# Kernel tuning notes

Hardware: AMD Instinct MI355X
Metric: run time of the kernel (lower is better)

Reference implementation:

```python
import jax, jax.numpy as jnp
import numpy as np

N = 50000

def gcn_conv(x, src, dst, W, b):
    # PyG GCNConv: h = x @ W; symmetric norm with self-loops; out = Ahat h + b
    h = x @ W  # [N, F]
    e = src.shape[0]
    deg = jax.ops.segment_sum(jnp.ones((e,), h.dtype), dst, num_segments=N) + 1.0  # +1 self-loop
    dinv = jax.lax.rsqrt(deg)  # deg >= 1 so finite
    norm = dinv[src] * dinv[dst]  # [E]
    agg = jax.ops.segment_sum(h[src] * norm[:, None], dst, num_segments=N)
    agg = agg + h * (dinv * dinv)[:, None]  # self-loop contribution
    return agg + b


def setup_inputs() -> dict:
    key = jax.random.key(0)
    ks = jax.random.split(key, 12)
    E = 400000
    x = jax.random.normal(ks[0], (N, 768), dtype=jnp.float32)
    edge_index = jax.random.randint(ks[1], (2, E), 0, N, dtype=jnp.int32)
    dims = [(768, 1536), (1536, 768), (768, 384), (384, 192), (192, 5)]
    inp = {"x": x, "edge_index": edge_index}
    for i, (fi, fo) in enumerate(dims):
        s = 1.0 / np.sqrt(fi)
        inp[f"W{i+1}"] = jax.random.uniform(ks[2 + 2 * i], (fi, fo), jnp.float32, -s, s)
        inp[f"b{i+1}"] = jnp.zeros((fo,), jnp.float32)
    return inp


def reference(x, edge_index, W1, b1, W2, b2, W3, b3, W4, b4, W5, b5):
    src, dst = edge_index[0], edge_index[1]
    h = x
    for W, b in [(W1, b1), (W2, b2), (W3, b3), (W4, b4)]:
        h = jax.nn.relu(gcn_conv(h, src, dst, W, b))
        # F.dropout with training=False is identity (eval mode)
    out = gcn_conv(h, src, dst, W5, b5)
    return (h, out)
```

## Files before the change

### kernel.cpp

```cpp
#include <hip/hip_runtime.h>
#include <stdint.h>

typedef unsigned short u16;
typedef unsigned int   u32;

#define NN 50000
#define NE 400000

typedef __bf16 bf16x8 __attribute__((ext_vector_type(8)));
typedef u16    u16x8  __attribute__((ext_vector_type(8)));
typedef float  f32x4  __attribute__((ext_vector_type(4)));

__device__ __forceinline__ float bf2f(u16 b) {
  union { u32 u; float f; } v; v.u = ((u32)b) << 16; return v.f;
}
__device__ __forceinline__ u16 f2bf(float f) {
  union { float f; u32 u; } v; v.f = f;
  u32 r = v.u + 0x7fffu + ((v.u >> 16) & 1u);
  return (u16)(r >> 16);
}


__global__ void zero_int_kernel(int* __restrict__ p, int n) {
  int i = blockIdx.x * blockDim.x + threadIdx.x;
  if (i < n) p[i] = 0;
}

__global__ void count_deg_kernel(const int* __restrict__ dst, int* __restrict__ deg, int e) {
  int i = blockIdx.x * blockDim.x + threadIdx.x;
  if (i < e) atomicAdd(&deg[dst[i]], 1);
}

__global__ void dinv_kernel(const int* __restrict__ deg, float* __restrict__ dinv, int n) {
  int i = blockIdx.x * blockDim.x + threadIdx.x;
  if (i < n) dinv[i] = rsqrtf((float)deg[i] + 1.0f);
}

__global__ __launch_bounds__(1024) void scan_kernel(const int* __restrict__ counts,
                                                    int* __restrict__ offsets, int n) {
  __shared__ int wsums[17];
  __shared__ int carry;
  int tid = threadIdx.x;
  int lane = tid & 63, wid = tid >> 6;
  if (tid == 0) carry = 0;
  __syncthreads();
  for (int base = 0; base < n; base += 1024) {
    int i = base + tid;
    int v = (i < n) ? counts[i] : 0;
    int s = v;
    #pragma unroll
    for (int off = 1; off < 64; off <<= 1) {
      int t = __shfl_up(s, off, 64);
      if (lane >= off) s += t;
    }
    if (lane == 63) wsums[wid] = s;
    __syncthreads();
    if (tid == 0) {
      int a = 0;
      #pragma unroll
      for (int w = 0; w < 16; ++w) { int t = wsums[w]; wsums[w] = a; a += t; }
      wsums[16] = a;
    }
    __syncthreads();
    if (i < n) offsets[i] = carry + wsums[wid] + s - v;
    __syncthreads();
    if (tid == 0) carry += wsums[16];
    __syncthreads();
  }
  if (tid == 0) offsets[n] = carry;
}

__global__ void csr_fill_kernel(const int* __restrict__ src, const int* __restrict__ dst,
                                const int* __restrict__ offsets, int* __restrict__ cursor,
                                const float* __restrict__ dinv,
                                int2* __restrict__ csr_pack, int e) {
  int i = blockIdx.x * blockDim.x + threadIdx.x;
  if (i < e) {
    int s = src[i], d = dst[i];
    int pos = offsets[d] + atomicAdd(&cursor[d], 1);
    float nr = dinv[s] * dinv[d];
    csr_pack[pos] = make_int2(s, __float_as_int(nr));
  }
}

__global__ void f2bf_kernel(const float* __restrict__ in, u16* __restrict__ out, int n) {
  int i = blockIdx.x * blockDim.x + threadIdx.x;
  if (i < n) out[i] = f2bf(in[i]);
}

__global__ void wt_kernel(const float* __restrict__ W, u16* __restrict__ Wt, int K, int N) {
  int i = blockIdx.x * blockDim.x + threadIdx.x;
  if (i < K * N) {
    int k = i / N;
    int n2 = i - k * N;
    Wt[n2 * K + k] = f2bf(W[i]);
  }
}


template<int G, bool HAS_BIAS, bool RELU, bool OUT_BF, bool OUT_F32>
__global__ __launch_bounds__(256) void agg8_kernel(
    const u16* __restrict__ g, const int* __restrict__ rowptr,
    const int2* __restrict__ csr_pack,
    const float* __restrict__ dinv, const float* __restrict__ bias,
    u16* __restrict__ outb, float* __restrict__ outf)
{
  constexpr int F = G * 8;
  int idx = blockIdx.x * blockDim.x + threadIdx.x;
  if (idx >= NN * G) return;
  int v = idx / G;
  int g8 = idx - v * G;
  const u16* base = g + g8 * 8;

  float acc[8];
  #pragma unroll
  for (int k = 0; k < 8; ++k) acc[k] = 0.f;

  int e0 = rowptr[v], e1 = rowptr[v + 1];
  int e = e0;
  for (; e + 3 < e1; e += 4) {
    int2 p0 = csr_pack[e];
    int2 p1 = csr_pack[e + 1];
    int2 p2 = csr_pack[e + 2];
    int2 p3 = csr_pack[e + 3];
    u16x8 r0 = *(const u16x8*)(base + (size_t)p0.x * F);
    u16x8 r1 = *(const u16x8*)(base + (size_t)p1.x * F);
    u16x8 r2 = *(const u16x8*)(base + (size_t)p2.x * F);
    u16x8 r3 = *(const u16x8*)(base + (size_t)p3.x * F);
    float n0 = __int_as_float(p0.y), n1 = __int_as_float(p1.y);
    float n2 = __int_as_float(p2.y), n3 = __int_as_float(p3.y);
    #pragma unroll
    for (int k = 0; k < 8; ++k) acc[k] += n0 * bf2f(r0[k]);
    #pragma unroll
    for (int k = 0; k < 8; ++k) acc[k] += n1 * bf2f(r1[k]);
    #pragma unroll
    for (int k = 0; k < 8; ++k) acc[k] += n2 * bf2f(r2[k]);
    #pragma unroll
    for (int k = 0; k < 8; ++k) acc[k] += n3 * bf2f(r3[k]);
  }
  for (; e < e1; ++e) {
    int2 p0 = csr_pack[e];
    u16x8 r0 = *(const u16x8*)(base + (size_t)p0.x * F);
    float n0 = __int_as_float(p0.y);
    #pragma unroll
    for (int k = 0; k < 8; ++k) acc[k] += n0 * bf2f(r0[k]);
  }

  float sv = dinv[v]; sv *= sv;
  u16x8 sr = *(const u16x8*)(base + (size_t)v * F);
  float vals[8];
  #pragma unroll
  for (int k = 0; k < 8; ++k) {
    float val = acc[k] + sv * bf2f(sr[k]);
    if (HAS_BIAS) val += bias[g8 * 8 + k];
    if (RELU) val = fmaxf(val, 0.f);
    vals[k] = val;
  }
  if (OUT_BF) {
    u16x8 ob;
    #pragma unroll
    for (int k = 0; k < 8; ++k) ob[k] = f2bf(vals[k]);
    *(u16x8*)(outb + (size_t)v * F + g8 * 8) = ob;
  }
  if (OUT_F32) {
    f32x4 o0, o1;
    #pragma unroll
    for (int k = 0; k < 4; ++k) { o0[k] = vals[k]; o1[k] = vals[4 + k]; }
    float* op = outf + (size_t)v * F + g8 * 8;
    *(f32x4*)op = o0;
    *(f32x4*)(op + 4) = o1;
  }
}

__global__ void agg_small_kernel(const u16* __restrict__ g, const int* __restrict__ rowptr,
                                 const int2* __restrict__ csr_pack,
                                 const float* __restrict__ dinv, const float* __restrict__ bias,
                                 float* __restrict__ out, int n, int F) {
  int idx = blockIdx.x * blockDim.x + threadIdx.x;
  if (idx >= n * F) return;
  int v = idx / F;
  int f = idx - v * F;
  float acc = 0.f;
  int e1 = rowptr[v + 1];
  for (int e = rowptr[v]; e < e1; ++e) {
    int2 p = csr_pack[e];
    acc += __int_as_float(p.y) * bf2f(g[p.x * F + f]);
  }
  float dv = dinv[v];
  out[idx] = acc + dv * dv * bf2f(g[v * F + f]) + bias[f];
}

#define WAIT_VMCNT4 0x0F74
#define WAIT_VMCNT0 0x0F70

__device__ __forceinline__ void gl_lds16(const void* g, void* l) {
  __builtin_amdgcn_global_load_lds((const __attribute__((address_space(1))) void*)g,
                                   (__attribute__((address_space(3))) void*)l, 16, 0, 0);
}


template<bool BIAS_RELU>
__global__ __launch_bounds__(512, 2) void gemm256_kernel(
    const u16* __restrict__ A, const u16* __restrict__ Bt,
    u16* __restrict__ C, const float* __restrict__ bias,
    int M, int N, int K)
{
  __shared__ __align__(16) u16 sA[2][2][256 * 32];
  __shared__ __align__(16) u16 sB[2][2][256 * 32];

  int gm = (M + 255) >> 8;
  int gn = (N + 255) >> 8;
  int bid = blockIdx.x;
  int xcd = bid & 7;
  int t = bid >> 3;
  int trow = t / gn;
  int bn_i = t - trow * gn;
  int rowt = trow * 8 + xcd;
  if (rowt >= gm) return;
  int bm = rowt << 8, bn = bn_i << 8;

  int tid = threadIdx.x;
  int wid = tid >> 6, lane = tid & 63;
  int wm = wid >> 2, wn = wid & 3;
  int row16 = lane & 15, q = lane >> 4;

  int sr = tid >> 2;
  int sq_log = ((tid & 3) - ((tid >> 3) & 3)) & 3;
  int ar0 = min(bm + sr, M - 1);
  int ar1 = min(bm + 128 + sr, M - 1);
  int br0 = min(bn + sr, N - 1);
  int br1 = min(bn + 128 + sr, N - 1);
  const u16* Ag0 = A + (size_t)ar0 * K + sq_log * 8;
  const u16* Ag1 = A + (size_t)ar1 * K + sq_log * 8;
  const u16* Bg0 = Bt + (size_t)br0 * K + sq_log * 8;
  const u16* Bg1 = Bt + (size_t)br1 * K + sq_log * 8;

  f32x4 acc[8][4];
  #pragma unroll
  for (int m = 0; m < 8; ++m)
    #pragma unroll
    for (int n = 0; n < 4; ++n)
      acc[m][n] = (f32x4){0.f, 0.f, 0.f, 0.f};

  auto stageA = [&](int nb, int h, int ko) {
    gl_lds16(Ag0 + ko, &sA[nb][h][tid * 8]);
    gl_lds16(Ag1 + ko, &sA[nb][h][4096 + tid * 8]);
  };
  auto stageB = [&](int nb, int h, int ko) {
    gl_lds16(Bg0 + ko, &sB[nb][h][tid * 8]);
    gl_lds16(Bg1 + ko, &sB[nb][h][4096 + tid * 8]);
  };

  stageA(0, 0, 0);
  stageB(0, 0, 0);
  stageA(0, 1, 32);
  stageB(0, 1, 32);
  __builtin_amdgcn_s_waitcnt(WAIT_VMCNT4);
  __builtin_amdgcn_s_barrier();

  const int KT = K >> 6;
  int perm = (q + (row16 >> 1)) & 3;
  int arow = (wm * 128 + row16) * 32 + perm * 8;
  int brow = (wn * 64 + row16) * 32 + perm * 8;

  for (int kt = 0; kt < KT; ++kt) {
    int buf = kt & 1, nb = buf ^ 1;
    bool pf = (kt + 1 < KT);
    int ko = (kt + 1) * 64;

    bf16x8 af[4], bfr[4];

    #pragma unroll
    for (int m = 0; m < 4; ++m) af[m] = *(const bf16x8*)&sA[buf][0][arow + m * 512];
    #pragma unroll
    for (int n = 0; n < 4; ++n) bfr[n] = *(const bf16x8*)&sB[buf][0][brow + n * 512];
    if (pf) stageA(nb, 0, ko);
    __builtin_amdgcn_s_setprio(1);
    #pragma unroll
    for (int m = 0; m < 4; ++m)
      #pragma unroll
      for (int n = 0; n < 4; ++n)
        acc[m][n] = __builtin_amdgcn_mfma_f32_16x16x32_bf16(af[m], bfr[n], acc[m][n], 0, 0, 0);
    __builtin_amdgcn_s_setprio(0);

    #pragma unroll
    for (int m = 0; m < 4; ++m) af[m] = *(const bf16x8*)&sA[buf][0][arow + (m + 4) * 512];
    if (pf) stageB(nb, 0, ko);
    __builtin_amdgcn_s_setprio(1);
    #pragma unroll
    for (int m = 0; m < 4; ++m)
      #pragma unroll
      for (int n = 0; n < 4; ++n)
        acc[m + 4][n] = __builtin_amdgcn_mfma_f32_16x16x32_bf16(af[m], bfr[n], acc[m + 4][n], 0, 0, 0);
    __builtin_amdgcn_s_setprio(0);

    if (pf) __builtin_amdgcn_s_waitcnt(WAIT_VMCNT4);
    else    __builtin_amdgcn_s_waitcnt(WAIT_VMCNT0);
    __builtin_amdgcn_s_barrier();

    #pragma unroll
    for (int m = 0; m < 4; ++m) af[m] = *(const bf16x8*)&sA[buf][1][arow + m * 512];
    #pragma unroll
    for (int n = 0; n < 4; ++n) bfr[n] = *(const bf16x8*)&sB[buf][1][brow + n * 512];
    if (pf) stageA(nb, 1, ko + 32);
    __builtin_amdgcn_s_setprio(1);
    #pragma unroll
    for (int m = 0; m < 4; ++m)
      #pragma unroll
      for (int n = 0; n < 4; ++n)
        acc[m][n] = __builtin_amdgcn_mfma_f32_16x16x32_bf16(af[m], bfr[n], acc[m][n], 0, 0, 0);
    __builtin_amdgcn_s_setprio(0);

    #pragma unroll
    for (int m = 0; m < 4; ++m) af[m] = *(const bf16x8*)&sA[buf][1][arow + (m + 4) * 512];
    if (pf) stageB(nb, 1, ko + 32);
    __builtin_amdgcn_s_setprio(1);
    #pragma unroll
    for (int m = 0; m < 4; ++m)
      #pragma unroll
      for (int n = 0; n < 4; ++n)
        acc[m + 4][n] = __builtin_amdgcn_mfma_f32_16x16x32_bf16(af[m], bfr[n], acc[m + 4][n], 0, 0, 0);
    __builtin_amdgcn_s_setprio(0);

    if (pf) {
      __builtin_amdgcn_s_waitcnt(WAIT_VMCNT4);
      __builtin_amdgcn_s_barrier();
    }
  }

  #pragma unroll
  for (int m = 0; m < 8; ++m) {
    int rbase = bm + wm * 128 + m * 16 + q * 4;
    #pragma unroll
    for (int n = 0; n < 4; ++n) {
      int col = bn + wn * 64 + n * 16 + row16;
      if (col < N) {
        float bv = BIAS_RELU ? bias[col] : 0.f;
        #pragma unroll
        for (int r = 0; r < 4; ++r) {
          int gr = rbase + r;
          if (gr < M) {
            float val = acc[m][n][r];
            if (BIAS_RELU) { val += bv; val = fmaxf(val, 0.f); }
            C[(size_t)gr * N + col] = f2bf(val);
          }
        }
      }
    }
  }
}

static inline int gemm256_grid(int M, int N) {
  int gm = (M + 255) / 256;
  int gn = (N + 255) / 256;
  int rows_per_xcd = (gm + 7) / 8;
  return rows_per_xcd * 8 * gn;
}


#define BM 128
#define BN 128
#define BK 32

template<bool BIAS_RELU>
__global__ __launch_bounds__(256, 4) void gemm_bt_kernel(
    const u16* __restrict__ A, const u16* __restrict__ Bt,
    u16* __restrict__ C, const float* __restrict__ bias,
    int M, int N, int K)
{
  __shared__ __align__(16) u16 As[2][BM * BK];
  __shared__ __align__(16) u16 Bs[2][BN * BK];
  int gm = (M + BM - 1) / BM;
  int gn = (N + BN - 1) / BN;
  int bid = blockIdx.x;
  int xcd = bid & 7;
  int t = bid >> 3;
  int trow = t / gn;
  int bn_i = t - trow * gn;
  int row = trow * 8 + xcd;
  if (row >= gm) return;
  int bm = row * BM, bn = bn_i * BN;

  int tid = threadIdx.x;
  int wave = tid >> 6, lane = tid & 63;
  int wm = wave & 1, wn = wave >> 1;

  int srow = tid >> 2;
  int sq_log = ((tid & 3) - ((tid >> 3) & 3)) & 3;
  int ar0 = min(bm + srow, M - 1);
  int ar1 = min(bm + 64 + srow, M - 1);
  int br0 = min(bn + srow, N - 1);
  int br1 = min(bn + 64 + srow, N - 1);
  const u16* ag0 = A + (size_t)ar0 * K + sq_log * 8;
  const u16* ag1 = A + (size_t)ar1 * K + sq_log * 8;
  const u16* bg0 = Bt + (size_t)br0 * K + sq_log * 8;
  const u16* bg1 = Bt + (size_t)br1 * K + sq_log * 8;
  int la0 = (wave * 16) * BK;
  int la1 = (64 + wave * 16) * BK;

  f32x4 acc[4][4];
  #pragma unroll
  for (int i = 0; i < 4; ++i)
    #pragma unroll
    for (int j = 0; j < 4; ++j)
      acc[i][j] = (f32x4){0.f, 0.f, 0.f, 0.f};

  int row16 = lane & 15, q = lane >> 4;
  int perm = (q + (row16 >> 1)) & 3;
  int ard = (wm * 64 + row16) * BK + perm * 8;
  int brd = (wn * 64 + row16) * BK + perm * 8;

  const int iters = K / BK;

  gl_lds16(ag0, &As[0][la0]);
  gl_lds16(ag1, &As[0][la1]);
  gl_lds16(bg0, &Bs[0][la0]);
  gl_lds16(bg1, &Bs[0][la1]);

  int buf = 0;
  for (int it = 0; it < iters; ++it) {
    __builtin_amdgcn_s_barrier();
    if (it + 1 < iters) {
      int kn = (it + 1) * BK;
      gl_lds16(ag0 + kn, &As[buf ^ 1][la0]);
      gl_lds16(ag1 + kn, &As[buf ^ 1][la1]);
      gl_lds16(bg0 + kn, &Bs[buf ^ 1][la0]);
      gl_lds16(bg1 + kn, &Bs[buf ^ 1][la1]);
      __builtin_amdgcn_s_waitcnt(WAIT_VMCNT4);
    } else {
      __builtin_amdgcn_s_waitcnt(WAIT_VMCNT0);
    }
    __builtin_amdgcn_s_barrier();

    bf16x8 af[4], bfr[4];
    #pragma unroll
    for (int i = 0; i < 4; ++i) af[i] = *(const bf16x8*)(&As[buf][ard + i * 16 * BK]);
    #pragma unroll
    for (int j = 0; j < 4; ++j) bfr[j] = *(const bf16x8*)(&Bs[buf][brd + j * 16 * BK]);
    #pragma unroll
    for (int i = 0; i < 4; ++i)
      #pragma unroll
      for (int j = 0; j < 4; ++j)
        acc[i][j] = __builtin_amdgcn_mfma_f32_16x16x32_bf16(af[i], bfr[j], acc[i][j], 0, 0, 0);
    buf ^= 1;
  }

  #pragma unroll
  for (int i = 0; i < 4; ++i) {
    int rbase = bm + wm * 64 + i * 16 + q * 4;
    #pragma unroll
    for (int j = 0; j < 4; ++j) {
      int col = bn + wn * 64 + j * 16 + row16;
      if (col < N) {
        float bv = BIAS_RELU ? bias[col] : 0.f;
        #pragma unroll
        for (int r = 0; r < 4; ++r) {
          int gr = rbase + r;
          if (gr < M) {
            float val = acc[i][j][r];
            if (BIAS_RELU) { val += bv; val = fmaxf(val, 0.f); }
            C[(size_t)gr * N + col] = f2bf(val);
          }
        }
      }
    }
  }
}

static inline int gemm_grid(int M, int N) {
  int gm = (M + BM - 1) / BM;
  int gn = (N + BN - 1) / BN;
  int rows_per_xcd = (gm + 7) / 8;
  return rows_per_xcd * gn * 8;
}


extern "C" void kernel_launch(void* const* d_in, const int* in_sizes, int n_in,
                              void* d_out, int out_size, void* d_ws, size_t ws_size,
                              hipStream_t stream) {
  const float* x   = (const float*)d_in[0];
  const int* ei    = (const int*)d_in[1];
  const int* src   = ei;
  const int* dst   = ei + NE;
  const float* W1  = (const float*)d_in[2];
  const float* b1  = (const float*)d_in[3];
  const float* W2  = (const float*)d_in[4];
  const float* b2  = (const float*)d_in[5];
  const float* W3  = (const float*)d_in[6];
  const float* b3  = (const float*)d_in[7];
  const float* W4  = (const float*)d_in[8];
  const float* b4  = (const float*)d_in[9];
  const float* W5  = (const float*)d_in[10];
  const float* b5  = (const float*)d_in[11];
  float* out_h = (float*)d_out;
  float* out_o = (float*)d_out + (size_t)NN * 192;

  char* p = (char*)d_ws;
  auto alloc = [&](size_t bytes) { char* r = p; p += (bytes + 255) & ~(size_t)255; return r; };
  int*   deg      = (int*)alloc((size_t)NN * 4);
  int*   cursor   = (int*)alloc((size_t)NN * 4);
  float* dinv     = (float*)alloc((size_t)NN * 4);
  int*   offs     = (int*)alloc((size_t)(NN + 1) * 4);
  int2*  csr_pack = (int2*)alloc((size_t)NE * 8);
  u16* W1t = (u16*)alloc((size_t)768 * 1536 * 2);
  u16* W2t = (u16*)alloc((size_t)1536 * 768 * 2);
  u16* W3t = (u16*)alloc((size_t)768 * 384 * 2);
  u16* W4t = (u16*)alloc((size_t)384 * 192 * 2);
  u16* W5t = (u16*)alloc((size_t)192 * 5 * 2);
  u16* B0 = (u16*)alloc((size_t)NN * 768 * 2);
  u16* B1 = (u16*)alloc((size_t)NN * 768 * 2);
  u16* B2 = (u16*)alloc((size_t)NN * 1536 * 2);

  u16* xb  = B0;
  u16* a0  = B1;
  u16* h1  = B2;
  u16* g2  = B0;
  u16* h2  = B1;
  u16* g3  = B0;
  u16* h3  = B2;
  u16* g4  = B0;
  u16* h4b = B1;
  u16* g5  = B0;

  const int M = NN;

  zero_int_kernel<<<(NN + 255) / 256, 256, 0, stream>>>(deg, NN);
  zero_int_kernel<<<(NN + 255) / 256, 256, 0, stream>>>(cursor, NN);
  count_deg_kernel<<<(NE + 255) / 256, 256, 0, stream>>>(dst, deg, NE);
  dinv_kernel<<<(NN + 255) / 256, 256, 0, stream>>>(deg, dinv, NN);
  scan_kernel<<<1, 1024, 0, stream>>>(deg, offs, NN);
  csr_fill_kernel<<<(NE + 255) / 256, 256, 0, stream>>>(src, dst, offs, cursor, dinv,
                                                        csr_pack, NE);
  f2bf_kernel<<<((NN * 768) + 255) / 256, 256, 0, stream>>>(x, xb, NN * 768);
  wt_kernel<<<((768 * 1536) + 255) / 256, 256, 0, stream>>>(W1, W1t, 768, 1536);
  wt_kernel<<<((1536 * 768) + 255) / 256, 256, 0, stream>>>(W2, W2t, 1536, 768);
  wt_kernel<<<((768 * 384) + 255) / 256, 256, 0, stream>>>(W3, W3t, 768, 384);
  wt_kernel<<<((384 * 192) + 255) / 256, 256, 0, stream>>>(W4, W4t, 384, 192);
  wt_kernel<<<((192 * 5) + 255) / 256, 256, 0, stream>>>(W5, W5t, 192, 5);

  dim3 blk(256);

  agg8_kernel<96, false, false, true, false><<<(NN * 96 + 255) / 256, blk, 0, stream>>>(
      xb, offs, csr_pack, dinv, nullptr, a0, nullptr);
  gemm256_kernel<true><<<gemm256_grid(M, 1536), 512, 0, stream>>>(
      a0, W1t, h1, b1, M, 1536, 768);

  gemm256_kernel<false><<<gemm256_grid(M, 768), 512, 0, stream>>>(
      h1, W2t, g2, nullptr, M, 768, 1536);
  agg8_kernel<96, true, true, true, false><<<(NN * 96 + 255) / 256, blk, 0, stream>>>(
      g2, offs, csr_pack, dinv, b2, h2, nullptr);

  gemm_bt_kernel<false><<<gemm_grid(M, 384), blk, 0, stream>>>(
      h2, W3t, g3, nullptr, M, 384, 768);
  agg8_kernel<48, true, true, true, false><<<(NN * 48 + 255) / 256, blk, 0, stream>>>(
      g3, offs, csr_pack, dinv, b3, h3, nullptr);

  gemm_bt_kernel<false><<<gemm_grid(M, 192), blk, 0, stream>>>(
      h3, W4t, g4, nullptr, M, 192, 384);
  agg8_kernel<24, true, true, true, true><<<(NN * 24 + 255) / 256, blk, 0, stream>>>(
      g4, offs, csr_pack, dinv, b4, h4b, out_h);

  gemm_bt_kernel<false><<<gemm_grid(M, 5), blk, 0, stream>>>(
      h4b, W5t, g5, nullptr, M, 5, 192);
  agg_small_kernel<<<((NN * 5) + 255) / 256, 256, 0, stream>>>(
      g5, offs, csr_pack, dinv, b5, out_o, NN, 5);
}
```

Baseline: 1.105 ms.

## Restructure GEMM LDS pipeline into 4-stage ring with K=32 steps

Replaces the double-buffered 64-wide K tile (two 32-wide halves per buffer) with a four-slot ring of 32-wide K tiles, prefetching three tiles ahead. This keeps more global-to-LDS loads in flight to hide memory latency. It adds extra barriers around each MFMA group and halves the work per loop iteration, so synchronisation overhead rises. LDS usage per block is unchanged.

Result: slower. 1.137 ms (+2.9%).

```diff
diff --git a/kernel.cpp b/kernel.cpp
--- a/kernel.cpp
+++ b/kernel.cpp
@@ -190,6 +190,7 @@
   out[idx] = acc + dv * dv * bf2f(g[v * F + f]) + bias[f];
 }
 
+#define WAIT_VMCNT8 0x0F78
 #define WAIT_VMCNT4 0x0F74
 #define WAIT_VMCNT0 0x0F70
 
@@ -205,16 +206,16 @@
     u16* __restrict__ C, const float* __restrict__ bias,
     int M, int N, int K)
 {
-  __shared__ __align__(16) u16 sA[2][2][256 * 32];
-  __shared__ __align__(16) u16 sB[2][2][256 * 32];
+  __shared__ __align__(16) u16 sA[4][256 * 32];
+  __shared__ __align__(16) u16 sB[4][256 * 32];
 
   int gm = (M + 255) >> 8;
   int gn = (N + 255) >> 8;
   int bid = blockIdx.x;
   int xcd = bid & 7;
-  int t = bid >> 3;
-  int trow = t / gn;
-  int bn_i = t - trow * gn;
+  int t0 = bid >> 3;
+  int trow = t0 / gn;
+  int bn_i = t0 - trow * gn;
   int rowt = trow * 8 + xcd;
   if (rowt >= gm) return;
   int bm = rowt << 8, bn = bn_i << 8;
@@ -242,90 +243,65 @@
     for (int n = 0; n < 4; ++n)
       acc[m][n] = (f32x4){0.f, 0.f, 0.f, 0.f};
 
-  auto stageA = [&](int nb, int h, int ko) {
-    gl_lds16(Ag0 + ko, &sA[nb][h][tid * 8]);
-    gl_lds16(Ag1 + ko, &sA[nb][h][4096 + tid * 8]);
+  auto stageA = [&](int b, int kt) {
+    gl_lds16(Ag0 + kt * 32, &sA[b][tid * 8]);
+    gl_lds16(Ag1 + kt * 32, &sA[b][4096 + tid * 8]);
   };
-  auto stageB = [&](int nb, int h, int ko) {
-    gl_lds16(Bg0 + ko, &sB[nb][h][tid * 8]);
-    gl_lds16(Bg1 + ko, &sB[nb][h][4096 + tid * 8]);
+  auto stageB = [&](int b, int kt) {
+    gl_lds16(Bg0 + kt * 32, &sB[b][tid * 8]);
+    gl_lds16(Bg1 + kt * 32, &sB[b][4096 + tid * 8]);
   };
 
-  stageA(0, 0, 0);
-  stageB(0, 0, 0);
-  stageA(0, 1, 32);
-  stageB(0, 1, 32);
-  __builtin_amdgcn_s_waitcnt(WAIT_VMCNT4);
+  const int KT = K >> 5;
+
+  stageA(0, 0); stageB(0, 0);
+  stageA(1, 1); stageB(1, 1);
+  stageA(2, 2); stageB(2, 2);
+  __builtin_amdgcn_s_waitcnt(WAIT_VMCNT8);
   __builtin_amdgcn_s_barrier();
 
-  const int KT = K >> 6;
   int perm = (q + (row16 >> 1)) & 3;
   int arow = (wm * 128 + row16) * 32 + perm * 8;
   int brow = (wn * 64 + row16) * 32 + perm * 8;
 
-  for (int kt = 0; kt < KT; ++kt) {
-    int buf = kt & 1, nb = buf ^ 1;
-    bool pf = (kt + 1 < KT);
-    int ko = (kt + 1) * 64;
+  for (int t = 0; t < KT; ++t) {
+    int buf = t & 3;
+    bool pf = (t + 3 < KT);
+    int sb = (t + 3) & 3;
 
     bf16x8 af[4], bfr[4];
 
     #pragma unroll
-    for (int m = 0; m < 4; ++m) af[m] = *(const bf16x8*)&sA[buf][0][arow + m * 512];
-    #pragma unroll
-    for (int n = 0; n < 4; ++n) bfr[n] = *(const bf16x8*)&sB[buf][0][brow + n * 512];
-    if (pf) stageA(nb, 0, ko);
+    for (int i = 0; i < 4; ++i) af[i] = *(const bf16x8*)&sA[buf][arow + i * 512];
+    #pragma unroll
+    for (int n = 0; n < 4; ++n) bfr[n] = *(const bf16x8*)&sB[buf][brow + n * 512];
+    if (pf) stageA(sb, t + 3);
+    __builtin_amdgcn_s_barrier();
     __builtin_amdgcn_s_setprio(1);
     #pragma unroll
-    for (int m = 0; m < 4; ++m)
+    for (int i = 0; i < 4; ++i)
       #pragma unroll
       for (int n = 0; n < 4; ++n)
-        acc[m][n] = __builtin_amdgcn_mfma_f32_16x16x32_bf16(af[m], bfr[n], acc[m][n], 0, 0, 0);
+        acc[i][n] = __builtin_amdgcn_mfma_f32_16x16x32_bf16(af[i], bfr[n], acc[i][n], 0, 0, 0);
     __builtin_amdgcn_s_setprio(0);
-
-    #pragma unroll
-    for (int m = 0; m < 4; ++m) af[m] = *(const bf16x8*)&sA[buf][0][arow + (m + 4) * 512];
-    if (pf) stageB(nb, 0, ko);
+    __builtin_amdgcn_s_barrier();
+
+    #pragma unroll
+    for (int i = 0; i < 4; ++i) af[i] = *(const bf16x8*)&sA[buf][arow + (i + 4) * 512];
+    if (pf) stageB(sb, t + 3);
+    __builtin_amdgcn_s_barrier();
     __builtin_amdgcn_s_setprio(1);
     #pragma unroll
-    for (int m = 0; m < 4; ++m)
+    for (int i = 0; i < 4; ++i)
       #pragma unroll
       for (int n = 0; n < 4; ++n)
-        acc[m + 4][n] = __builtin_amdgcn_mfma_f32_16x16x32_bf16(af[m], bfr[n], acc[m + 4][n], 0, 0, 0);
+        acc[i + 4][n] = __builtin_amdgcn_mfma_f32_16x16x32_bf16(af[i], bfr[n], acc[i + 4][n], 0, 0, 0);
     __builtin_amdgcn_s_setprio(0);
 
-    if (pf) __builtin_amdgcn_s_waitcnt(WAIT_VMCNT4);
-    else    __builtin_amdgcn_s_waitcnt(WAIT_VMCNT0);
-    __builtin_amdgcn_s_barrier();
-
-    #pragma unroll
-    for (int m = 0; m < 4; ++m) af[m] = *(const bf16x8*)&sA[buf][1][arow + m * 512];
-    #pragma unroll
-    for (int n = 0; n < 4; ++n) bfr[n] = *(const bf16x8*)&sB[buf][1][brow + n * 512];
-    if (pf) stageA(nb, 1, ko + 32);
-    __builtin_amdgcn_s_setprio(1);
-    #pragma unroll
-    for (int m = 0; m < 4; ++m)
-      #pragma unroll
-      for (int n = 0; n < 4; ++n)
-        acc[m][n] = __builtin_amdgcn_mfma_f32_16x16x32_bf16(af[m], bfr[n], acc[m][n], 0, 0, 0);
-    __builtin_amdgcn_s_setprio(0);
-
-    #pragma unroll
-    for (int m = 0; m < 4; ++m) af[m] = *(const bf16x8*)&sA[buf][1][arow + (m + 4) * 512];
-    if (pf) stageB(nb, 1, ko + 32);
-    __builtin_amdgcn_s_setprio(1);
-    #pragma unroll
-    for (int m = 0; m < 4; ++m)
-      #pragma unroll
-      for (int n = 0; n < 4; ++n)
-        acc[m + 4][n] = __builtin_amdgcn_mfma_f32_16x16x32_bf16(af[m], bfr[n], acc[m + 4][n], 0, 0, 0);
-    __builtin_amdgcn_s_setprio(0);
-
-    if (pf) {
-      __builtin_amdgcn_s_waitcnt(WAIT_VMCNT4);
-      __builtin_amdgcn_s_barrier();
-    }
+    if (t < KT - 3)       __builtin_amdgcn_s_waitcnt(WAIT_VMCNT8);
+    else if (t == KT - 3) __builtin_amdgcn_s_waitcnt(WAIT_VMCNT4);
+    else if (t == KT - 2) __builtin_amdgcn_s_waitcnt(WAIT_VMCNT0);
+    if (t < KT - 1)       __builtin_amdgcn_s_barrier();
   }
 
   #pragma unroll
```
